# Kernel optimization log

Hardware: AMD Instinct MI355X
Metric: run time of the kernel (lower is better)

Reference implementation:

```python
import jax, jax.numpy as jnp
import numpy as np

N_NODES = 50000
N_EDGES = 800000
HID = 128
EDGE_IN = 2 * HID + 4 + 20  # 2*hidden + edge_feat_dim + num_r_gaussian = 280


def setup_inputs() -> dict:
    key = jax.random.key(0)
    ks = jax.random.split(key, 16)
    s = lambda fan_in: 1.0 / np.sqrt(fan_in)
    inp = {
        "h": jax.random.normal(ks[0], (N_NODES, HID), dtype=jnp.float32),
        "edge_index": jax.random.randint(ks[1], (2, N_EDGES), 0, N_NODES, dtype=jnp.int64) if jax.config.jax_enable_x64 else jax.random.randint(ks[1], (2, N_EDGES), 0, N_NODES, dtype=jnp.int32),
        "edge_attr": jax.random.normal(ks[2], (N_EDGES, 24), dtype=jnp.float32),
        # edge_mlp: Linear(280->128) relu Linear(128->128) relu (act_last=True)
        "We1": jax.random.uniform(ks[3], (EDGE_IN, HID), jnp.float32, -s(EDGE_IN), s(EDGE_IN)),
        "be1": jnp.zeros((HID,), jnp.float32),
        "We2": jax.random.uniform(ks[4], (HID, HID), jnp.float32, -s(HID), s(HID)),
        "be2": jnp.zeros((HID,), jnp.float32),
        # edge_inf: Linear(128->1) + sigmoid
        "Wg": jax.random.uniform(ks[5], (HID, 1), jnp.float32, -s(HID), s(HID)),
        "bg": jnp.zeros((1,), jnp.float32),
        # node_mlp: Linear(256->128) relu Linear(128->128)
        "Wn1": jax.random.uniform(ks[6], (2 * HID, HID), jnp.float32, -s(2 * HID), s(2 * HID)),
        "bn1": jnp.zeros((HID,), jnp.float32),
        "Wn2": jax.random.uniform(ks[7], (HID, HID), jnp.float32, -s(HID), s(HID)),
        "bn2": jnp.zeros((HID,), jnp.float32),
    }
    return inp


def reference(h, edge_index, edge_attr, We1, be1, We2, be2, Wg, bg, Wn1, bn1, Wn2, bn2):
    dst, src = edge_index[0], edge_index[1]
    hi, hj = h[dst], h[src]                       # [E, HID] each
    x = jnp.concatenate([edge_attr, hi, hj], -1)  # [E, 280]
    mij = jax.nn.relu(jax.nn.relu(x @ We1 + be1) @ We2 + be2)  # [E, HID]
    eij = jax.nn.sigmoid(mij @ Wg + bg)           # [E, 1]
    mi = jax.ops.segment_sum(mij * eij, dst, num_segments=h.shape[0])  # [N, HID]
    y = jnp.concatenate([mi, h], -1)              # [N, 2*HID]
    out = jax.nn.relu(y @ Wn1 + bn1) @ Wn2 + bn2  # [N, HID]
    return out
```

## Files before the change

kernel.cpp:

```cpp
#include <hip/hip_runtime.h>

#define N_NODES 50000
#define N_EDGES 800000
#define HID 128

typedef _Float16 f16;
typedef _Float16 half8 __attribute__((ext_vector_type(8)));
typedef _Float16 half4 __attribute__((ext_vector_type(4)));
typedef _Float16 half2v __attribute__((ext_vector_type(2)));
typedef float f32x4 __attribute__((ext_vector_type(4)));
typedef float f32x2 __attribute__((ext_vector_type(2)));

#define OFF_MI     0UL
#define OFF_H16C   25600000UL
#define OFF_WC     38400000UL
#define OFF_CNT    38604800UL
#define OFF_CUR    38805504UL
#define OFF_PERM   39006208UL
#define OFF_BT     42206208UL
#define CSR_TOTAL  42206464UL

#define OFF_FMI  0UL
#define OFF_FH16 25600000UL
#define OFF_FW   38400000UL

#define WB1 0
#define WB2 36864
#define WN1 53248
#define WN2 86016

#define TS 136
#define YS 264
#define AS 40

#define EB 32

__global__ __launch_bounds__(256) void pack_weights(
    const float* __restrict__ We1, const float* __restrict__ We2,
    const float* __restrict__ Wn1, const float* __restrict__ Wn2,
    f16* __restrict__ W, int* __restrict__ cnt) {
  int i = blockIdx.x * 256 + threadIdx.x;
  if (cnt && i < 50176) cnt[i] = 0;
  if (i < 36864) {
    int j = i & 7, n = (i >> 3) & 127, qk = i >> 10;
    int k = qk * 8 + j;
    float v = 0.f;
    if (k < 256) v = We1[(24 + k) * 128 + n];
    else if (k < 280) v = We1[(k - 256) * 128 + n];
    W[WB1 + i] = (f16)v;
  } else if (i < 53248) {
    int l = i - 36864;
    int j = l & 7, n = (l >> 3) & 127, qk = l >> 10;
    W[WB2 + l] = (f16)We2[(qk * 8 + j) * 128 + n];
  } else if (i < 86016) {
    int l = i - 53248;
    int j = l & 7, n = (l >> 3) & 127, qk = l >> 10;
    W[WN1 + l] = (f16)Wn1[(qk * 8 + j) * 128 + n];
  } else if (i < 102400) {
    int l = i - 86016;
    int j = l & 7, n = (l >> 3) & 127, qk = l >> 10;
    W[WN2 + l] = (f16)Wn2[(qk * 8 + j) * 128 + n];
  }
}

__global__ __launch_bounds__(256) void scanA(const int* __restrict__ cnt,
                                             int* __restrict__ cur, int* __restrict__ bt) {
  __shared__ int wsum[4];
  int t = threadIdx.x, b = blockIdx.x;
  int base = b * 1024 + t * 4;
  int4 v = *(const int4*)(cnt + base);
  int s = v.x + v.y + v.z + v.w;
  int lane = t & 63, w = t >> 6;
  int inc = s;
  #pragma unroll
  for (int off = 1; off < 64; off <<= 1) {
    int u = __shfl_up(inc, off, 64);
    if (lane >= off) inc += u;
  }
  if (lane == 63) wsum[w] = inc;
  __syncthreads();
  int wbase = 0;
  for (int i = 0; i < w; ++i) wbase += wsum[i];
  int excl = wbase + inc - s;
  int4 o;
  o.x = excl; o.y = excl + v.x; o.z = o.y + v.y; o.w = o.z + v.z;
  *(int4*)(cur + base) = o;
  if (t == 255) bt[b] = wbase + inc;
}

__global__ __launch_bounds__(64) void scanB(int* __restrict__ bt) {
  int l = threadIdx.x;
  int v = (l < 49) ? bt[l] : 0;
  int inc = v;
  #pragma unroll
  for (int off = 1; off < 64; off <<= 1) {
    int u = __shfl_up(inc, off, 64);
    if (l >= off) inc += u;
  }
  if (l < 49) bt[l] = inc - v;
}

__global__ __launch_bounds__(256) void scanC(int* __restrict__ cur, const int* __restrict__ bt) {
  int t = threadIdx.x, b = blockIdx.x;
  int base = b * 1024 + t * 4;
  int add = bt[b];
  int4 o = *(int4*)(cur + base);
  o.x += add; o.y += add; o.z += add; o.w += add;
  *(int4*)(cur + base) = o;
}

__global__ __launch_bounds__(256) void fill_perm(
    const int* __restrict__ eidx, int* __restrict__ cur, int* __restrict__ perm) {
  int i = blockIdx.x * 256 + threadIdx.x;
  int p = atomicAdd(&cur[eidx[i]], 1);
  perm[p] = i;
}

__global__ __launch_bounds__(256, 4) void precompute_kernel(
    const float* __restrict__ h, const int* __restrict__ eidx,
    const f16* __restrict__ Wp, f16* __restrict__ P,
    f16* __restrict__ h16, int* __restrict__ cnt) {
  __shared__ f16 Y[64 * 136];
  int t = threadIdx.x;
  int n0 = blockIdx.x * 64;
  {
    int rb = t >> 4, ch = t & 15;
    for (int p = 0; p < 4; ++p) {
      int r = p * 16 + rb;
      int g = n0 + r; if (g >= N_NODES) g = N_NODES - 1;
      const float4* s4 = (const float4*)(h + (size_t)g * HID + ch * 8);
      float4 a = s4[0], b = s4[1];
      half8 v = {(f16)a.x, (f16)a.y, (f16)a.z, (f16)a.w,
                 (f16)b.x, (f16)b.y, (f16)b.z, (f16)b.w};
      *(half8*)&Y[r * 136 + ch * 8] = v;
      *(half8*)(h16 + (size_t)g * HID + ch * 8) = v;
    }
  }
  if (cnt) {
    for (int i = blockIdx.x * 256 + t; i < N_EDGES; i += gridDim.x * 256)
      atomicAdd(&cnt[eidx[i]], 1);
  }
  __syncthreads();
  int w = t >> 6, lane = t & 63, q = lane >> 4, c = lane & 15;
  int colBase = w * 32;
  const f16* B = Wp + WB1 + ((size_t)(q * 128 + colBase + c)) * 8;
  f32x4 aD[4][2], aS[4][2];
  #pragma unroll
  for (int mt = 0; mt < 4; ++mt) {
    aD[mt][0] = (f32x4){0, 0, 0, 0}; aD[mt][1] = (f32x4){0, 0, 0, 0};
    aS[mt][0] = (f32x4){0, 0, 0, 0}; aS[mt][1] = (f32x4){0, 0, 0, 0};
  }
  #pragma unroll
  for (int ks = 0; ks < 4; ++ks) {
    half8 bD0 = *(const half8*)(B + ks * 4096);
    half8 bD1 = *(const half8*)(B + ks * 4096 + 128);
    half8 bS0 = *(const half8*)(B + (ks + 4) * 4096);
    half8 bS1 = *(const half8*)(B + (ks + 4) * 4096 + 128);
    #pragma unroll
    for (int mt = 0; mt < 4; ++mt) {
      half8 a = *(const half8*)&Y[(mt * 16 + c) * 136 + ks * 32 + q * 8];
      aD[mt][0] = __builtin_amdgcn_mfma_f32_16x16x32_f16(a, bD0, aD[mt][0], 0, 0, 0);
      aD[mt][1] = __builtin_amdgcn_mfma_f32_16x16x32_f16(a, bD1, aD[mt][1], 0, 0, 0);
      aS[mt][0] = __builtin_amdgcn_mfma_f32_16x16x32_f16(a, bS0, aS[mt][0], 0, 0, 0);
      aS[mt][1] = __builtin_amdgcn_mfma_f32_16x16x32_f16(a, bS1, aS[mt][1], 0, 0, 0);
    }
  }
  #pragma unroll
  for (int mt = 0; mt < 4; ++mt)
    #pragma unroll
    for (int r = 0; r < 4; ++r) {
      int g = n0 + mt * 16 + q * 4 + r;
      if (g < N_NODES) {
        f16* o = P + (size_t)g * 256 + colBase + c;
        o[0]        = (f16)aD[mt][0][r];
        o[16]       = (f16)aD[mt][1][r];
        o[128]      = (f16)aS[mt][0][r];
        o[128 + 16] = (f16)aS[mt][1][r];
      }
    }
}

__global__ __launch_bounds__(256, 8) void edge_kernel(
    const f16* __restrict__ P, const int* __restrict__ eidx,
    const float* __restrict__ eattr,
    const f16* __restrict__ Wp, const float* __restrict__ be1,
    const float* __restrict__ be2,
    const float* __restrict__ Wg, const float* __restrict__ bg,
    float* __restrict__ mi, const int* __restrict__ perm) {
  __shared__ f16 S16[EB * TS];
  __shared__ f16 A[EB * AS];
  __shared__ float part[EB * 4];
  __shared__ float eijL[EB];
  __shared__ int dstL[EB];
  int t = threadIdx.x;
  int e0 = blockIdx.x * EB;

  if (t < EB) {
    int e = perm ? perm[e0 + t] : (e0 + t);
    dstL[t] = eidx[e];
  }
  {
    int rb = t >> 4, ch = t & 15;
    for (int p = 0; p < 2; ++p) {
      int r = p * 16 + rb;
      int e = perm ? perm[e0 + r] : (e0 + r);
      int d = eidx[e];
      int s = eidx[N_EDGES + e];
      half8 pd = *(const half8*)(P + (size_t)d * 256 + ch * 8);
      half8 ps = *(const half8*)(P + (size_t)s * 256 + 128 + ch * 8);
      *(half8*)&S16[r * TS + ch * 8] = pd + ps;
    }
  }
  if (t < 192) {
    int el = t / 6, kk = t % 6;
    int e = perm ? perm[e0 + el] : (e0 + el);
    float4 f = *(const float4*)(eattr + (size_t)e * 24 + kk * 4);
    half4 hv = {(f16)f.x, (f16)f.y, (f16)f.z, (f16)f.w};
    *(half4*)&A[el * AS + kk * 4] = hv;
  }
  if (t < EB) { uint4 z = {0, 0, 0, 0}; *(uint4*)&A[t * AS + 24] = z; }
  __syncthreads();

  int w = t >> 6, lane = t & 63, q = lane >> 4, c = lane & 15;
  int colBase = w * 32;

  f32x4 acc[2][2];
  {
    float b0 = be1[colBase + c], b1 = be1[colBase + 16 + c];
    #pragma unroll
    for (int mt = 0; mt < 2; ++mt) {
      acc[mt][0] = (f32x4){b0, b0, b0, b0};
      acc[mt][1] = (f32x4){b1, b1, b1, b1};
    }
  }
  {
    const f16* bA = Wp + WB1 + 32768 + ((size_t)(q * 128 + colBase + c)) * 8;
    half8 b0f = *(const half8*)(bA);
    half8 b1f = *(const half8*)(bA + 128);
    #pragma unroll
    for (int mt = 0; mt < 2; ++mt) {
      half8 a = *(const half8*)&A[(mt * 16 + c) * AS + q * 8];
      acc[mt][0] = __builtin_amdgcn_mfma_f32_16x16x32_f16(a, b0f, acc[mt][0], 0, 0, 0);
      acc[mt][1] = __builtin_amdgcn_mfma_f32_16x16x32_f16(a, b1f, acc[mt][1], 0, 0, 0);
    }
  }
  #pragma unroll
  for (int mt = 0; mt < 2; ++mt)
    #pragma unroll
    for (int r = 0; r < 4; ++r) {
      const f16* sr = &S16[(mt * 16 + q * 4 + r) * TS + colBase + c];
      acc[mt][0][r] += (float)sr[0];
      acc[mt][1][r] += (float)sr[16];
    }

  const f16* bp2base = Wp + WB2 + ((size_t)(q * 128 + colBase + c)) * 8;
  half8 d0 = *(const half8*)(bp2base);
  half8 d1 = *(const half8*)(bp2base + 128);

  __syncthreads();
  f16* T = S16;
  #pragma unroll
  for (int mt = 0; mt < 2; ++mt)
    #pragma unroll
    for (int nt = 0; nt < 2; ++nt)
      #pragma unroll
      for (int r = 0; r < 4; ++r) {
        float v = acc[mt][nt][r];
        T[(mt * 16 + q * 4 + r) * TS + colBase + nt * 16 + c] = (f16)(v > 0.f ? v : 0.f);
      }
  __syncthreads();

  f32x4 m2[2][2];
  {
    float b0 = be2[colBase + c], b1 = be2[colBase + 16 + c];
    #pragma unroll
    for (int mt = 0; mt < 2; ++mt) {
      m2[mt][0] = (f32x4){b0, b0, b0, b0};
      m2[mt][1] = (f32x4){b1, b1, b1, b1};
    }
  }
  #pragma unroll
  for (int kk = 0; kk < 4; ++kk) {
    half8 n0, n1;
    if (kk < 3) {
      n0 = *(const half8*)(bp2base + (kk + 1) * 4096);
      n1 = *(const half8*)(bp2base + (kk + 1) * 4096 + 128);
    }
    #pragma unroll
    for (int mt = 0; mt < 2; ++mt) {
      half8 a = *(const half8*)&T[(mt * 16 + c) * TS + kk * 32 + q * 8];
      m2[mt][0] = __builtin_amdgcn_mfma_f32_16x16x32_f16(a, d0, m2[mt][0], 0, 0, 0);
      m2[mt][1] = __builtin_amdgcn_mfma_f32_16x16x32_f16(a, d1, m2[mt][1], 0, 0, 0);
    }
    d0 = n0; d1 = n1;
  }

  float wg0 = Wg[colBase + c], wg1 = Wg[colBase + 16 + c];
  float pd[2][4];
  #pragma unroll
  for (int mt = 0; mt < 2; ++mt)
    #pragma unroll
    for (int r = 0; r < 4; ++r) {
      float v0 = m2[mt][0][r]; v0 = v0 > 0.f ? v0 : 0.f; m2[mt][0][r] = v0;
      float v1 = m2[mt][1][r]; v1 = v1 > 0.f ? v1 : 0.f; m2[mt][1][r] = v1;
      pd[mt][r] = v0 * wg0 + v1 * wg1;
    }
  #pragma unroll
  for (int off = 1; off < 16; off <<= 1)
    #pragma unroll
    for (int mt = 0; mt < 2; ++mt)
      #pragma unroll
      for (int r = 0; r < 4; ++r)
        pd[mt][r] += __shfl_xor(pd[mt][r], off, 64);
  if (c == 0)
    #pragma unroll
    for (int mt = 0; mt < 2; ++mt)
      #pragma unroll
      for (int r = 0; r < 4; ++r)
        part[(mt * 16 + q * 4 + r) * 4 + w] = pd[mt][r];
  __syncthreads();
  if (t < EB) {
    float s = part[t * 4] + part[t * 4 + 1] + part[t * 4 + 2] + part[t * 4 + 3] + bg[0];
    eijL[t] = 1.f / (1.f + __expf(-s));
  }
  __syncthreads();

  if (perm) {
    #pragma unroll
    for (int mt = 0; mt < 2; ++mt)
      #pragma unroll
      for (int r = 0; r < 4; ++r) {
        int el = mt * 16 + q * 4 + r;
        float ev = eijL[el];
        T[el * TS + colBase + c]      = (f16)(m2[mt][0][r] * ev);
        T[el * TS + colBase + 16 + c] = (f16)(m2[mt][1][r] * ev);
      }
    __syncthreads();
    int col = t & 127, half = t >> 7;
    int r0 = half * 16;
    float acc2 = 0.f;
    int dprev = dstL[r0];
    #pragma unroll
    for (int r2 = 0; r2 < 16; ++r2) {
      int rr = r0 + r2;
      acc2 += (float)T[rr * TS + col];
      int dnext = (r2 == 15) ? -1 : dstL[rr + 1];
      if (dnext != dprev) {
        atomicAdd(&mi[(size_t)dprev * HID + col], acc2);
        acc2 = 0.f;
        dprev = dnext;
      }
    }
  } else {
    #pragma unroll
    for (int mt = 0; mt < 2; ++mt)
      #pragma unroll
      for (int r = 0; r < 4; ++r) {
        int el = mt * 16 + q * 4 + r;
        float ev = eijL[el];
        float* base = mi + (size_t)dstL[el] * HID + colBase + c;
        atomicAdd(base,      m2[mt][0][r] * ev);
        atomicAdd(base + 16, m2[mt][1][r] * ev);
      }
  }
}

__global__ __launch_bounds__(256, 4) void node_kernel(
    const float* __restrict__ mi, const f16* __restrict__ h16,
    const f16* __restrict__ Wp, const float* __restrict__ bn1,
    const float* __restrict__ bn2, float* __restrict__ out) {
  __shared__ f16 Y[64 * YS];
  int t = threadIdx.x;
  int n0 = blockIdx.x * 64;
  {
    int rb = t >> 4, ch = t & 15;
    for (int p = 0; p < 4; ++p) {
      int r = p * 16 + rb;
      int g = n0 + r; if (g >= N_NODES) g = N_NODES - 1;
      const float4* s = (const float4*)(mi + (size_t)g * HID + ch * 8);
      float4 a = s[0], b = s[1];
      half8 v = {(f16)a.x, (f16)a.y, (f16)a.z, (f16)a.w,
                 (f16)b.x, (f16)b.y, (f16)b.z, (f16)b.w};
      *(half8*)&Y[r * YS + ch * 8] = v;
      *(uint4*)&Y[r * YS + 128 + ch * 8] = *(const uint4*)(h16 + (size_t)g * HID + ch * 8);
    }
  }
  __syncthreads();
  int w = t >> 6, lane = t & 63, q = lane >> 4, c = lane & 15;
  int colBase = w * 32;
  const f16* BN1 = Wp + WN1;
  const f16* BN2 = Wp + WN2;
  f32x4 acc[4][2];
  {
    float b0 = bn1[colBase + c], b1 = bn1[colBase + 16 + c];
    #pragma unroll
    for (int mt = 0; mt < 4; ++mt) {
      acc[mt][0] = (f32x4){b0, b0, b0, b0};
      acc[mt][1] = (f32x4){b1, b1, b1, b1};
    }
  }
  const f16* bn1base = BN1 + ((size_t)(q * 128 + colBase + c)) * 8;
  half8 bf0 = *(const half8*)(bn1base);
  half8 bf1 = *(const half8*)(bn1base + 128);
  #pragma unroll
  for (int ks = 0; ks < 8; ++ks) {
    half8 nb0, nb1;
    if (ks < 7) {
      nb0 = *(const half8*)(bn1base + (ks + 1) * 4096);
      nb1 = *(const half8*)(bn1base + (ks + 1) * 4096 + 128);
    }
    #pragma unroll
    for (int mt = 0; mt < 4; ++mt) {
      half8 a = *(const half8*)&Y[(mt * 16 + c) * YS + ks * 32 + q * 8];
      acc[mt][0] = __builtin_amdgcn_mfma_f32_16x16x32_f16(a, bf0, acc[mt][0], 0, 0, 0);
      acc[mt][1] = __builtin_amdgcn_mfma_f32_16x16x32_f16(a, bf1, acc[mt][1], 0, 0, 0);
    }
    bf0 = nb0; bf1 = nb1;
  }
  const f16* bn2base = BN2 + ((size_t)(q * 128 + colBase + c)) * 8;
  half8 d0 = *(const half8*)(bn2base);
  half8 d1 = *(const half8*)(bn2base + 128);
  __syncthreads();
  f16* T = Y;
  #pragma unroll
  for (int mt = 0; mt < 4; ++mt)
    #pragma unroll
    for (int nt = 0; nt < 2; ++nt)
      #pragma unroll
      for (int r = 0; r < 4; ++r) {
        float v = acc[mt][nt][r];
        T[(mt * 16 + q * 4 + r) * TS + colBase + nt * 16 + c] = (f16)(v > 0.f ? v : 0.f);
      }
  __syncthreads();
  f32x4 m2[4][2];
  {
    float b0 = bn2[colBase + c], b1 = bn2[colBase + 16 + c];
    #pragma unroll
    for (int mt = 0; mt < 4; ++mt) {
      m2[mt][0] = (f32x4){b0, b0, b0, b0};
      m2[mt][1] = (f32x4){b1, b1, b1, b1};
    }
  }
  #pragma unroll
  for (int kk = 0; kk < 4; ++kk) {
    half8 n0, n1;
    if (kk < 3) {
      n0 = *(const half8*)(bn2base + (kk + 1) * 4096);
      n1 = *(const half8*)(bn2base + (kk + 1) * 4096 + 128);
    }
    #pragma unroll
    for (int mt = 0; mt < 4; ++mt) {
      half8 a = *(const half8*)&T[(mt * 16 + c) * TS + kk * 32 + q * 8];
      m2[mt][0] = __builtin_amdgcn_mfma_f32_16x16x32_f16(a, d0, m2[mt][0], 0, 0, 0);
      m2[mt][1] = __builtin_amdgcn_mfma_f32_16x16x32_f16(a, d1, m2[mt][1], 0, 0, 0);
    }
    d0 = n0; d1 = n1;
  }
  #pragma unroll
  for (int mt = 0; mt < 4; ++mt)
    #pragma unroll
    for (int r = 0; r < 4; ++r) {
      int g = n0 + mt * 16 + q * 4 + r;
      if (g < N_NODES) {
        float* o = out + (size_t)g * HID + colBase + c;
        o[0]  = m2[mt][0][r];
        o[16] = m2[mt][1][r];
      }
    }
}

extern "C" void kernel_launch(void* const* d_in, const int* in_sizes, int n_in,
                              void* d_out, int out_size, void* d_ws, size_t ws_size,
                              hipStream_t stream) {
  const float* h    = (const float*)d_in[0];
  const int*   eidx = (const int*)d_in[1];
  const float* eattr= (const float*)d_in[2];
  const float* We1  = (const float*)d_in[3];
  const float* be1  = (const float*)d_in[4];
  const float* We2  = (const float*)d_in[5];
  const float* be2  = (const float*)d_in[6];
  const float* Wg   = (const float*)d_in[7];
  const float* bg   = (const float*)d_in[8];
  const float* Wn1  = (const float*)d_in[9];
  const float* bn1  = (const float*)d_in[10];
  const float* Wn2  = (const float*)d_in[11];
  const float* bn2  = (const float*)d_in[12];
  float* out = (float*)d_out;
  char* ws = (char*)d_ws;

  if (ws_size >= CSR_TOTAL) {
    float* mi  = (float*)(ws + OFF_MI);
    f16* h16   = (f16*)(ws + OFF_H16C);
    f16* Wp    = (f16*)(ws + OFF_WC);
    int* cnt   = (int*)(ws + OFF_CNT);
    int* cur   = (int*)(ws + OFF_CUR);
    int* perm  = (int*)(ws + OFF_PERM);
    int* bt    = (int*)(ws + OFF_BT);
    f16* P     = (f16*)out;

    hipMemsetAsync(mi, 0, (size_t)N_NODES * HID * sizeof(float), stream);
    pack_weights<<<400, 256, 0, stream>>>(We1, We2, Wn1, Wn2, Wp, cnt);
    precompute_kernel<<<(N_NODES + 63) / 64, 256, 0, stream>>>(h, eidx, Wp, P, h16, cnt);
    scanA<<<49, 256, 0, stream>>>(cnt, cur, bt);
    scanB<<<1, 64, 0, stream>>>(bt);
    scanC<<<49, 256, 0, stream>>>(cur, bt);
    fill_perm<<<3125, 256, 0, stream>>>(eidx, cur, perm);
    edge_kernel<<<N_EDGES / EB, 256, 0, stream>>>(P, eidx, eattr, Wp, be1, be2,
                                                  Wg, bg, mi, perm);
    node_kernel<<<(N_NODES + 63) / 64, 256, 0, stream>>>(mi, h16, Wp, bn1, bn2, out);
  } else {
    float* mi  = (float*)(ws + OFF_FMI);
    f16*   h16 = (f16*)(ws + OFF_FH16);
    f16*   Wp  = (f16*)(ws + OFF_FW);
    f16*   P   = (f16*)out;

    hipMemsetAsync(mi, 0, (size_t)N_NODES * HID * sizeof(float), stream);
    pack_weights<<<400, 256, 0, stream>>>(We1, We2, Wn1, Wn2, Wp, nullptr);
    precompute_kernel<<<(N_NODES + 63) / 64, 256, 0, stream>>>(h, eidx, Wp, P, h16, nullptr);
    edge_kernel<<<N_EDGES / EB, 256, 0, stream>>>(P, eidx, eattr, Wp, be1, be2,
                                                  Wg, bg, mi, nullptr);
    node_kernel<<<(N_NODES + 63) / 64, 256, 0, stream>>>(mi, h16, Wp, bn1, bn2, out);
  }
}
```

Baseline: 404.6 us.

## Store sorted edge records with endpoints, fold memset and block scan into neighbours

fill_perm now writes a 16-byte record (edge id, dst, src) per sorted slot, so the edge kernel reads endpoints contiguously instead of doing a dependent gather through perm into edge_index. The separate memset of mi is folded into pack_weights, and scanB is removed by having each scanC block reduce the preceding block totals itself. This cuts two launches and a level of indirect loads, in exchange for a larger workspace and heavier fill_perm stores.

```diff
diff --git a/kernel.cpp b/kernel.cpp
--- a/kernel.cpp
+++ b/kernel.cpp
@@ -16,9 +16,9 @@
 #define OFF_WC     38400000UL
 #define OFF_CNT    38604800UL
 #define OFF_CUR    38805504UL
-#define OFF_PERM   39006208UL
-#define OFF_BT     42206208UL
-#define CSR_TOTAL  42206464UL
+#define OFF_E4     39006208UL
+#define OFF_BT     51806208UL
+#define CSR_TOTAL  51806464UL
 
 #define OFF_FMI  0UL
 #define OFF_FH16 25600000UL
@@ -38,9 +38,14 @@
 __global__ __launch_bounds__(256) void pack_weights(
     const float* __restrict__ We1, const float* __restrict__ We2,
     const float* __restrict__ Wn1, const float* __restrict__ Wn2,
-    f16* __restrict__ W, int* __restrict__ cnt) {
+    f16* __restrict__ W, int* __restrict__ cnt, float* __restrict__ mi) {
   int i = blockIdx.x * 256 + threadIdx.x;
   if (cnt && i < 50176) cnt[i] = 0;
+  if (mi) {
+    f32x4 z = {0.f, 0.f, 0.f, 0.f};
+    for (int j = i; j < N_NODES * HID / 4; j += 102400)
+      ((f32x4*)mi)[j] = z;
+  }
   if (i < 36864) {
     int j = i & 7, n = (i >> 3) & 127, qk = i >> 10;
     int k = qk * 8 + j;
@@ -88,32 +93,31 @@
   if (t == 255) bt[b] = wbase + inc;
 }
 
-__global__ __launch_bounds__(64) void scanB(int* __restrict__ bt) {
-  int l = threadIdx.x;
-  int v = (l < 49) ? bt[l] : 0;
-  int inc = v;
-  #pragma unroll
-  for (int off = 1; off < 64; off <<= 1) {
-    int u = __shfl_up(inc, off, 64);
-    if (l >= off) inc += u;
-  }
-  if (l < 49) bt[l] = inc - v;
-}
-
 __global__ __launch_bounds__(256) void scanC(int* __restrict__ cur, const int* __restrict__ bt) {
+  __shared__ int sbase;
   int t = threadIdx.x, b = blockIdx.x;
+  if (t < 64) {
+    int v = (t < b) ? bt[t] : 0;
+    #pragma unroll
+    for (int off = 32; off; off >>= 1) v += __shfl_down(v, off, 64);
+    if (t == 0) sbase = v;
+  }
+  __syncthreads();
+  int add = sbase;
   int base = b * 1024 + t * 4;
-  int add = bt[b];
   int4 o = *(int4*)(cur + base);
   o.x += add; o.y += add; o.z += add; o.w += add;
   *(int4*)(cur + base) = o;
 }
 
 __global__ __launch_bounds__(256) void fill_perm(
-    const int* __restrict__ eidx, int* __restrict__ cur, int* __restrict__ perm) {
+    const int* __restrict__ eidx, int* __restrict__ cur, int4* __restrict__ e4) {
   int i = blockIdx.x * 256 + threadIdx.x;
-  int p = atomicAdd(&cur[eidx[i]], 1);
-  perm[p] = i;
+  int d = eidx[i];
+  int s = eidx[N_EDGES + i];
+  int p = atomicAdd(&cur[d], 1);
+  int4 rec; rec.x = i; rec.y = d; rec.z = s; rec.w = 0;
+  e4[p] = rec;
 }
 
 __global__ __launch_bounds__(256, 4) void precompute_kernel(
@@ -186,7 +190,7 @@
     const f16* __restrict__ Wp, const float* __restrict__ be1,
     const float* __restrict__ be2,
     const float* __restrict__ Wg, const float* __restrict__ bg,
-    float* __restrict__ mi, const int* __restrict__ perm) {
+    float* __restrict__ mi, const int4* __restrict__ e4) {
   __shared__ f16 S16[EB * TS];
   __shared__ f16 A[EB * AS];
   __shared__ float part[EB * 4];
@@ -195,17 +199,19 @@
   int t = threadIdx.x;
   int e0 = blockIdx.x * EB;
 
-  if (t < EB) {
-    int e = perm ? perm[e0 + t] : (e0 + t);
-    dstL[t] = eidx[e];
-  }
+  if (t < EB) dstL[t] = e4 ? e4[e0 + t].y : eidx[e0 + t];
+
   {
     int rb = t >> 4, ch = t & 15;
     for (int p = 0; p < 2; ++p) {
       int r = p * 16 + rb;
-      int e = perm ? perm[e0 + r] : (e0 + r);
-      int d = eidx[e];
-      int s = eidx[N_EDGES + e];
+      int d, s;
+      if (e4) {
+        int4 rec = e4[e0 + r];
+        d = rec.y; s = rec.z;
+      } else {
+        d = eidx[e0 + r]; s = eidx[N_EDGES + e0 + r];
+      }
       half8 pd = *(const half8*)(P + (size_t)d * 256 + ch * 8);
       half8 ps = *(const half8*)(P + (size_t)s * 256 + 128 + ch * 8);
       *(half8*)&S16[r * TS + ch * 8] = pd + ps;
@@ -213,7 +219,7 @@
   }
   if (t < 192) {
     int el = t / 6, kk = t % 6;
-    int e = perm ? perm[e0 + el] : (e0 + el);
+    int e = e4 ? e4[e0 + el].x : (e0 + el);
     float4 f = *(const float4*)(eattr + (size_t)e * 24 + kk * 4);
     half4 hv = {(f16)f.x, (f16)f.y, (f16)f.z, (f16)f.w};
     *(half4*)&A[el * AS + kk * 4] = hv;
@@ -325,7 +331,7 @@
   }
   __syncthreads();
 
-  if (perm) {
+  if (e4) {
     #pragma unroll
     for (int mt = 0; mt < 2; ++mt)
       #pragma unroll
@@ -494,19 +500,17 @@
     f16* Wp    = (f16*)(ws + OFF_WC);
     int* cnt   = (int*)(ws + OFF_CNT);
     int* cur   = (int*)(ws + OFF_CUR);
-    int* perm  = (int*)(ws + OFF_PERM);
+    int4* e4   = (int4*)(ws + OFF_E4);
     int* bt    = (int*)(ws + OFF_BT);
     f16* P     = (f16*)out;
 
-    hipMemsetAsync(mi, 0, (size_t)N_NODES * HID * sizeof(float), stream);
-    pack_weights<<<400, 256, 0, stream>>>(We1, We2, Wn1, Wn2, Wp, cnt);
+    pack_weights<<<400, 256, 0, stream>>>(We1, We2, Wn1, Wn2, Wp, cnt, mi);
     precompute_kernel<<<(N_NODES + 63) / 64, 256, 0, stream>>>(h, eidx, Wp, P, h16, cnt);
     scanA<<<49, 256, 0, stream>>>(cnt, cur, bt);
-    scanB<<<1, 64, 0, stream>>>(bt);
     scanC<<<49, 256, 0, stream>>>(cur, bt);
-    fill_perm<<<3125, 256, 0, stream>>>(eidx, cur, perm);
+    fill_perm<<<3125, 256, 0, stream>>>(eidx, cur, e4);
     edge_kernel<<<N_EDGES / EB, 256, 0, stream>>>(P, eidx, eattr, Wp, be1, be2,
-                                                  Wg, bg, mi, perm);
+                                                  Wg, bg, mi, e4);
     node_kernel<<<(N_NODES + 63) / 64, 256, 0, stream>>>(mi, h16, Wp, bn1, bn2, out);
   } else {
     float* mi  = (float*)(ws + OFF_FMI);
@@ -514,8 +518,7 @@
     f16*   Wp  = (f16*)(ws + OFF_FW);
     f16*   P   = (f16*)out;
 
-    hipMemsetAsync(mi, 0, (size_t)N_NODES * HID * sizeof(float), stream);
-    pack_weights<<<400, 256, 0, stream>>>(We1, We2, Wn1, Wn2, Wp, nullptr);
+    pack_weights<<<400, 256, 0, stream>>>(We1, We2, Wn1, Wn2, Wp, nullptr, mi);
     precompute_kernel<<<(N_NODES + 63) / 64, 256, 0, stream>>>(h, eidx, Wp, P, h16, nullptr);
     edge_kernel<<<N_EDGES / EB, 256, 0, stream>>>(P, eidx, eattr, Wp, be1, be2,
                                                   Wg, bg, mi, nullptr);
```

New measurement: 391.8 us. 1.03x faster.
